# Kernel tuning notes

Hardware: AMD Instinct MI355X
Metric: run time of the kernel (lower is better)

## Reference

```python
import jax, jax.numpy as jnp
import numpy as np

HEADS = 8
HEAD_DIM = 64
SCALE = HEAD_DIM ** -0.5


def setup_inputs() -> dict:
    key = jax.random.key(0)
    ks = jax.random.split(key, 5)
    d_model, inner = 1024, HEADS * HEAD_DIM  # 512
    x = jax.random.normal(ks[0], (2, 2048, d_model), dtype=jnp.float32)
    # torch Linear weights stored pre-transposed as [in, out]
    Wq = jax.random.normal(ks[1], (d_model, inner), dtype=jnp.float32) * (d_model ** -0.5)
    Wkv = jax.random.normal(ks[2], (d_model, 2 * inner), dtype=jnp.float32) * (d_model ** -0.5)
    Wo = jax.random.normal(ks[3], (inner, d_model), dtype=jnp.float32) * (inner ** -0.5)
    bo = jnp.zeros((d_model,), dtype=jnp.float32)
    return {"x": x, "Wq": Wq, "Wkv": Wkv, "Wo": Wo, "bo": bo}


def reference(x, Wq, Wkv, Wo, bo):
    b, n, _ = x.shape
    q = x @ Wq                       # [b, n, h*d]
    kv = x @ Wkv                     # [b, n, 2*h*d] (self-attention: context = x)
    k, v = jnp.split(kv, 2, axis=-1)

    def split_heads(t):
        return t.reshape(b, n, HEADS, HEAD_DIM).transpose(0, 2, 1, 3)  # [b, h, n, d]

    q, k, v = map(split_heads, (q, k, v))
    sim = jnp.einsum('bhid,bhjd->bhij', q, k) * SCALE  # [b, h, n, n]
    attn = jax.nn.softmax(sim, axis=-1)                # dropout p=0.0 -> identity
    out = jnp.einsum('bhij,bhjd->bhid', attn, v)       # [b, h, n, d]
    out = out.transpose(0, 2, 1, 3).reshape(b, n, HEADS * HEAD_DIM)
    return out @ Wo + bo
```

## Files before the change

### kernel.cpp

```cpp
#include <hip/hip_runtime.h>

typedef _Float16 f16;
typedef __attribute__((ext_vector_type(4))) _Float16 f16x4;
typedef __attribute__((ext_vector_type(8))) _Float16 f16x8;
typedef __attribute__((ext_vector_type(4))) float f32x4;

#define CEXP 0.18033688011112042f
#define QKB_LD 1056

__device__ __forceinline__ void gload16(const f16* g, f16* l) {
    __builtin_amdgcn_global_load_lds((const __attribute__((address_space(1))) void*)g,
                                     (__attribute__((address_space(3))) void*)l, 16, 0, 0);
}

__global__ __launch_bounds__(256) void conv_f32_f16_k(const float* __restrict__ in,
                                                      f16* __restrict__ out) {
    int idx = (blockIdx.x * 256 + threadIdx.x) * 8;
    float4 a = *(const float4*)(in + idx);
    float4 b = *(const float4*)(in + idx + 4);
    f16x8 o;
    o[0] = (f16)a.x; o[1] = (f16)a.y; o[2] = (f16)a.z; o[3] = (f16)a.w;
    o[4] = (f16)b.x; o[5] = (f16)b.y; o[6] = (f16)b.z; o[7] = (f16)b.w;
    *(f16x8*)(out + idx) = o;
}

__global__ __launch_bounds__(256) void transpose_conv_k(const float* __restrict__ in,
                                                        f16* __restrict__ out,
                                                        int N, int ldo, int row_off) {
    __shared__ float tile[32][33];
    int tx = threadIdx.x & 31, ty = threadIdx.x >> 5;
    int n0 = blockIdx.x * 32, k0 = blockIdx.y * 32;
#pragma unroll
    for (int j = 0; j < 4; j++)
        tile[ty + j * 8][tx] = in[(size_t)(k0 + ty + j * 8) * N + n0 + tx];
    __syncthreads();
#pragma unroll
    for (int j = 0; j < 4; j++)
        out[(size_t)(row_off + n0 + ty + j * 8) * ldo + k0 + tx] = (f16)tile[tx][ty + j * 8];
}

template <int MODE, int BN>
__global__ __launch_bounds__(256) void gemm_k(
    const f16* __restrict__ A, const f16* __restrict__ Bt,
    f16* __restrict__ Cqk, f16* __restrict__ Cvt,
    float* __restrict__ Cout, const float* __restrict__ bias,
    int K, int NTILES) {
    __shared__ __align__(16) f16 As[128 * 64];
    __shared__ __align__(16) f16 Bs[BN * 64];
    constexpr int MI = (BN == 128) ? 4 : 2;
    int bid = blockIdx.x;
    int nt = bid % NTILES, mt = bid / NTILES;
    int m0 = mt * 128, n0 = nt * BN;
    int tid = threadIdx.x;
    int lane = tid & 63, w = tid >> 6;
    int rowBase = (BN == 128) ? (w >> 1) * 64 : w * 32;
    int colBase = (BN == 128) ? (w & 1) * 64 : 0;
    int lr = lane & 15, lg = lane >> 4;
    int rowL = lane >> 3;
    int colL = (lane & 7) * 8;
    int bRow0 = (BN == 128) ? w * 32 : w * 16;
    const f16* aSrc = A + (size_t)(m0 + w * 32 + rowL) * K + colL;
    const f16* bSrc = Bt + (size_t)(n0 + bRow0 + rowL) * K + colL;
    f32x4 acc[MI][4] = {};

    for (int k0 = 0; k0 < K; k0 += 64) {
#pragma unroll
        for (int j = 0; j < 4; j++)
            gload16(aSrc + k0 + (size_t)(j * 8) * K, &As[(w * 32 + j * 8) * 64]);
#pragma unroll
        for (int j = 0; j < (BN == 128 ? 4 : 2); j++)
            gload16(bSrc + k0 + (size_t)(j * 8) * K, &Bs[(bRow0 + j * 8) * 64]);
        __syncthreads();
#pragma unroll
        for (int ks = 0; ks < 2; ks++) {
            f16x8 af[MI], bf[4];
#pragma unroll
            for (int i = 0; i < MI; i++)
                af[i] = *(const f16x8*)(&As[(rowBase + i * 16 + lr) * 64 + ks * 32 + lg * 8]);
#pragma unroll
            for (int j = 0; j < 4; j++)
                bf[j] = *(const f16x8*)(&Bs[(colBase + j * 16 + lr) * 64 + ks * 32 + lg * 8]);
#pragma unroll
            for (int i = 0; i < MI; i++)
#pragma unroll
                for (int j = 0; j < 4; j++)
                    acc[i][j] = __builtin_amdgcn_mfma_f32_16x16x32_f16(af[i], bf[j], acc[i][j], 0, 0, 0);
        }
        __syncthreads();
    }

#pragma unroll
    for (int i = 0; i < MI; i++) {
#pragma unroll
        for (int j = 0; j < 4; j++) {
            int row = m0 + rowBase + i * 16 + lg * 4;
            int col = n0 + colBase + j * 16 + lr;
            if (MODE == 1) {
                float bv = bias[col];
#pragma unroll
                for (int r = 0; r < 4; r++)
                    Cout[(size_t)(row + r) * 1024 + col] = acc[i][j][r] + bv;
            } else {
                if (col < 1024) {
                    float sc = (col < 512) ? CEXP : 1.0f;
#pragma unroll
                    for (int r = 0; r < 4; r++)
                        Cqk[(size_t)(row + r) * QKB_LD + col] = (f16)(acc[i][j][r] * sc);
                } else {
                    int c = col - 1024;
                    int hh = c >> 6, d = c & 63;
                    int bb = row >> 11, n = row & 2047;
                    int pr = bb * 8 + hh;
                    int tt = n >> 6, kvl = n & 63;
                    int kg = kvl >> 4, lga = (kvl >> 2) & 3;
                    int dgp = d >> 5, dh = (d >> 4) & 1, lra = d & 15;
                    f16x4 ov;
#pragma unroll
                    for (int r = 0; r < 4; r++) ov[r] = (f16)acc[i][j][r];
                    size_t idx = ((((size_t)(pr * 32 + tt) * 4 + kg) * 2 + dgp) * 64
                                  + lga * 16 + lra) * 8 + dh * 4;
                    *(f16x4*)(Cvt + idx) = ov;
                }
            }
        }
    }
}

__global__ __launch_bounds__(512, 4) void attn_k(const f16* __restrict__ qkb,
                                                 const f16* __restrict__ vt2,
                                                 f16* __restrict__ ao) {
    __shared__ __align__(16) f16 Ks[2][4 * 4096];

    int bid = blockIdx.x;
    int xcd = bid & 7;
    int pair = xcd * 2 + ((bid >> 3) & 1);
    int qblk = bid >> 4;
    int b = pair >> 3, h = pair & 7;
    int tid = threadIdx.x;
    int lane = tid & 63, w = tid >> 6;
    int half = w >> 2, wl = w & 3;
    int lr = lane & 15, lg = lane >> 4;
    int q0 = qblk * 64 + wl * 16;

    const f16* qb = qkb + (size_t)b * 2048 * QKB_LD + h * 64;
    const f16* kb = qb + 512;

    f16x8 qf0 = *(const f16x8*)(qb + (size_t)(q0 + lr) * QKB_LD + lg * 8);
    f16x8 qf1 = *(const f16x8*)(qb + (size_t)(q0 + lr) * QKB_LD + 32 + lg * 8);

    int srcCol = (((lane & 7) ^ (lane >> 3)) << 3);
    int rowL = lane >> 3;
    const f16* ksrc = kb + (size_t)(half * 1024 + wl * 16 + rowL) * QKB_LD + srcCol;
    const f16* vbase = vt2 + ((size_t)pair * 32) * 4096 + lane * 8;

    auto stageK = [&](int buf, int tt) {
        f16* dst = &Ks[half][buf * 4096 + (wl * 16) * 64];
        gload16(ksrc + (size_t)(tt * 64) * QKB_LD, dst);
        gload16(ksrc + (size_t)(tt * 64 + 8) * QKB_LD, dst + 8 * 64);
    };

    stageK(0, 0); stageK(1, 1); stageK(2, 2);
    asm volatile("s_waitcnt vmcnt(2)" ::: "memory");
    __builtin_amdgcn_s_barrier();
    asm volatile("" ::: "memory");

    int kOffA = (lg * 8) ^ ((lr & 7) << 3);

    f32x4 acc[4] = {};
    float m = -INFINITY, lp = 0.f;
    f32x4 sA[4], sB[4];

    {
        __builtin_amdgcn_s_setprio(1);
#pragma unroll
        for (int kg = 0; kg < 4; kg++) {
            const f16* krow = &Ks[half][(kg * 16 + lr) * 64];
            f16x8 ka0 = *(const f16x8*)(krow + kOffA);
            f16x8 ka1 = *(const f16x8*)(krow + (kOffA ^ 32));
            f32x4 z = {};
            z = __builtin_amdgcn_mfma_f32_16x16x32_f16(ka0, qf0, z, 0, 0, 0);
            sA[kg] = __builtin_amdgcn_mfma_f32_16x16x32_f16(ka1, qf1, z, 0, 0, 0);
        }
        __builtin_amdgcn_s_setprio(0);
    }

    auto body = [&](f32x4 (&sCur)[4], f32x4 (&sNxt)[4], int t) {
        const f16* vl = vbase + (size_t)(half * 16 + t) * 4096;
        f16x8 vv[8];
#pragma unroll
        for (int i = 0; i < 8; i++) vv[i] = *(const f16x8*)(vl + i * 512);

        if (t <= 12) stageK((t + 3) & 3, t + 3);

        if (t < 15) {
            const f16* kbuf = &Ks[half][((t + 1) & 3) * 4096];
            __builtin_amdgcn_s_setprio(1);
#pragma unroll
            for (int kg = 0; kg < 4; kg++) {
                const f16* krow = kbuf + (kg * 16 + lr) * 64;
                f16x8 ka0 = *(const f16x8*)(krow + kOffA);
                f16x8 ka1 = *(const f16x8*)(krow + (kOffA ^ 32));
                f32x4 z = {};
                z = __builtin_amdgcn_mfma_f32_16x16x32_f16(ka0, qf0, z, 0, 0, 0);
                sNxt[kg] = __builtin_amdgcn_mfma_f32_16x16x32_f16(ka1, qf1, z, 0, 0, 0);
            }
            __builtin_amdgcn_s_setprio(0);
        }

        float x0 = fmaxf(fmaxf(sCur[0][0], sCur[0][1]), fmaxf(sCur[0][2], sCur[0][3]));
        float x1 = fmaxf(fmaxf(sCur[1][0], sCur[1][1]), fmaxf(sCur[1][2], sCur[1][3]));
        float x2 = fmaxf(fmaxf(sCur[2][0], sCur[2][1]), fmaxf(sCur[2][2], sCur[2][3]));
        float x3 = fmaxf(fmaxf(sCur[3][0], sCur[3][1]), fmaxf(sCur[3][2], sCur[3][3]));
        float ownmx = fmaxf(fmaxf(x0, x1), fmaxf(x2, x3));
        if (!__all(ownmx - m <= 8.f)) {
            float mx = fmaxf(ownmx, __shfl_xor(ownmx, 16, 64));
            mx = fmaxf(mx, __shfl_xor(mx, 32, 64));
            float mn = fmaxf(m, mx);
            float alpha = __builtin_amdgcn_exp2f(m - mn);
            m = mn;
            lp *= alpha;
#pragma unroll
            for (int dg = 0; dg < 4; dg++)
#pragma unroll
                for (int r = 0; r < 4; r++) acc[dg][r] *= alpha;
        }
        f16x4 pf[4];
#pragma unroll
        for (int kg = 0; kg < 4; kg++) {
            float p0 = __builtin_amdgcn_exp2f(sCur[kg][0] - m);
            float p1 = __builtin_amdgcn_exp2f(sCur[kg][1] - m);
            float p2 = __builtin_amdgcn_exp2f(sCur[kg][2] - m);
            float p3 = __builtin_amdgcn_exp2f(sCur[kg][3] - m);
            pf[kg][0] = (f16)p0; pf[kg][1] = (f16)p1;
            pf[kg][2] = (f16)p2; pf[kg][3] = (f16)p3;
            lp += (p0 + p1) + (p2 + p3);
        }

        __builtin_amdgcn_s_setprio(1);
#pragma unroll
        for (int kg = 0; kg < 4; kg++)
#pragma unroll
            for (int dgp = 0; dgp < 2; dgp++) {
                f16x8 vx = vv[kg * 2 + dgp];
                f16x4 vlo = __builtin_shufflevector(vx, vx, 0, 1, 2, 3);
                f16x4 vhi = __builtin_shufflevector(vx, vx, 4, 5, 6, 7);
                acc[dgp * 2]     = __builtin_amdgcn_mfma_f32_16x16x16f16(vlo, pf[kg], acc[dgp * 2], 0, 0, 0);
                acc[dgp * 2 + 1] = __builtin_amdgcn_mfma_f32_16x16x16f16(vhi, pf[kg], acc[dgp * 2 + 1], 0, 0, 0);
            }
        __builtin_amdgcn_s_setprio(0);

        if (t <= 12)      { asm volatile("s_waitcnt vmcnt(2)" ::: "memory"); }
        else if (t == 13) { asm volatile("s_waitcnt vmcnt(0)" ::: "memory"); }
        if (t < 15) {
            __builtin_amdgcn_s_barrier();
            asm volatile("" ::: "memory");
        }
    };

    for (int u = 0; u < 8; u++) {
        body(sA, sB, 2 * u);
        body(sB, sA, 2 * u + 1);
    }

    lp += __shfl_xor(lp, 16, 64);
    lp += __shfl_xor(lp, 32, 64);
    __syncthreads();
    float* mO = (float*)&Ks[0][0];
    float* mL = mO + 4 * 64 * 16;
    float* mM = mL + 4 * 64;
    if (half == 1) {
#pragma unroll
        for (int dg = 0; dg < 4; dg++)
            *(f32x4*)&mO[(wl * 64 + lane) * 16 + dg * 4] = acc[dg];
        mL[wl * 64 + lane] = lp;
        mM[wl * 64 + lane] = m;
    }
    __syncthreads();
    if (half == 0) {
        float mP = mM[wl * 64 + lane];
        float lpP = mL[wl * 64 + lane];
        float M = fmaxf(m, mP);
        float a = __builtin_amdgcn_exp2f(m - M);
        float c = __builtin_amdgcn_exp2f(mP - M);
        float inv = 1.f / (lp * a + lpP * c);
#pragma unroll
        for (int dg = 0; dg < 4; dg++) {
            f32x4 oP = *(const f32x4*)&mO[(wl * 64 + lane) * 16 + dg * 4];
            f16x4 ov;
#pragma unroll
            for (int r = 0; r < 4; r++)
                ov[r] = (f16)((acc[dg][r] * a + oP[r] * c) * inv);
            *(f16x4*)(ao + (size_t)(b * 2048 + q0 + lr) * 512 + h * 64 + dg * 16 + lg * 4) = ov;
        }
    }
}

extern "C" void kernel_launch(void* const* d_in, const int* in_sizes, int n_in,
                              void* d_out, int out_size, void* d_ws, size_t ws_size,
                              hipStream_t stream) {
    const float* x   = (const float*)d_in[0];
    const float* Wq  = (const float*)d_in[1];
    const float* Wkv = (const float*)d_in[2];
    const float* Wo  = (const float*)d_in[3];
    const float* bo  = (const float*)d_in[4];
    float* out = (float*)d_out;

    f16* xb    = (f16*)d_ws;
    f16* wqkvT = xb + 4096 * 1024;
    f16* woT   = wqkvT + 1536 * 1024;
    f16* qkb   = woT + 1024 * 512;
    f16* vtb2  = qkb + 4096 * QKB_LD;
    f16* ao    = vtb2 + 16 * 32 * 4096;

    conv_f32_f16_k<<<2048, 256, 0, stream>>>(x, xb);
    transpose_conv_k<<<dim3(16, 32), 256, 0, stream>>>(Wq, wqkvT, 512, 1024, 0);
    transpose_conv_k<<<dim3(32, 32), 256, 0, stream>>>(Wkv, wqkvT, 1024, 1024, 512);
    transpose_conv_k<<<dim3(32, 16), 256, 0, stream>>>(Wo, woT, 1024, 512, 0);

    gemm_k<0, 64><<<32 * 24, 256, 0, stream>>>(xb, wqkvT, qkb, vtb2, nullptr, nullptr, 1024, 24);
    attn_k<<<512, 512, 0, stream>>>(qkb, vtb2, ao);
    gemm_k<1, 128><<<32 * 8, 256, 0, stream>>>(ao, woT, nullptr, nullptr, out, bo, 512, 8);
}
```

Baseline: 92.34 us.

## Double-buffer GEMM LDS tiles and restructure attention K staging into 128-row blocks

The GEMM kernel gets double-buffered LDS tiles, so the next K-slice loads while the current one is multiplied. This hides global-to-LDS latency behind MFMA work. The attention kernel replaces its 4-deep 64-row K ring and software-pipelined QK^T with a 2-buffer scheme that stages 128 keys per iteration and computes both 64-key score blocks up front. That halves the number of barriers, but it drops the cross-iteration overlap of QK^T with softmax, relies on __syncthreads (full vmcnt waits) and raises register pressure.

Result: slower. 96.89 us (+4.9%).

```diff
diff --git a/kernel.cpp b/kernel.cpp
--- a/kernel.cpp
+++ b/kernel.cpp
@@ -45,9 +45,10 @@
     f16* __restrict__ Cqk, f16* __restrict__ Cvt,
     float* __restrict__ Cout, const float* __restrict__ bias,
     int K, int NTILES) {
-    __shared__ __align__(16) f16 As[128 * 64];
-    __shared__ __align__(16) f16 Bs[BN * 64];
+    __shared__ __align__(16) f16 As[2][128 * 64];
+    __shared__ __align__(16) f16 Bs[2][BN * 64];
     constexpr int MI = (BN == 128) ? 4 : 2;
+    constexpr int NB = (BN == 128) ? 4 : 2;
     int bid = blockIdx.x;
     int nt = bid % NTILES, mt = bid / NTILES;
     int m0 = mt * 128, n0 = nt * BN;
@@ -63,23 +64,31 @@
     const f16* bSrc = Bt + (size_t)(n0 + bRow0 + rowL) * K + colL;
     f32x4 acc[MI][4] = {};
 
-    for (int k0 = 0; k0 < K; k0 += 64) {
+    auto stage = [&](int buf, int k0) {
 #pragma unroll
         for (int j = 0; j < 4; j++)
-            gload16(aSrc + k0 + (size_t)(j * 8) * K, &As[(w * 32 + j * 8) * 64]);
-#pragma unroll
-        for (int j = 0; j < (BN == 128 ? 4 : 2); j++)
-            gload16(bSrc + k0 + (size_t)(j * 8) * K, &Bs[(bRow0 + j * 8) * 64]);
-        __syncthreads();
+            gload16(aSrc + k0 + (size_t)(j * 8) * K, &As[buf][(w * 32 + j * 8) * 64]);
+#pragma unroll
+        for (int j = 0; j < NB; j++)
+            gload16(bSrc + k0 + (size_t)(j * 8) * K, &Bs[buf][(bRow0 + j * 8) * 64]);
+    };
+
+    stage(0, 0);
+    __syncthreads();
+
+    int KT = K >> 6;
+    for (int kt = 0; kt < KT; kt++) {
+        int cur = kt & 1;
+        if (kt + 1 < KT) stage(cur ^ 1, (kt + 1) * 64);
 #pragma unroll
         for (int ks = 0; ks < 2; ks++) {
             f16x8 af[MI], bf[4];
 #pragma unroll
             for (int i = 0; i < MI; i++)
-                af[i] = *(const f16x8*)(&As[(rowBase + i * 16 + lr) * 64 + ks * 32 + lg * 8]);
+                af[i] = *(const f16x8*)(&As[cur][(rowBase + i * 16 + lr) * 64 + ks * 32 + lg * 8]);
 #pragma unroll
             for (int j = 0; j < 4; j++)
-                bf[j] = *(const f16x8*)(&Bs[(colBase + j * 16 + lr) * 64 + ks * 32 + lg * 8]);
+                bf[j] = *(const f16x8*)(&Bs[cur][(colBase + j * 16 + lr) * 64 + ks * 32 + lg * 8]);
 #pragma unroll
             for (int i = 0; i < MI; i++)
 #pragma unroll
@@ -129,7 +138,7 @@
 __global__ __launch_bounds__(512, 4) void attn_k(const f16* __restrict__ qkb,
                                                  const f16* __restrict__ vt2,
                                                  f16* __restrict__ ao) {
-    __shared__ __align__(16) f16 Ks[2][4 * 4096];
+    __shared__ __align__(16) f16 Ks[2][2][128 * 64];
 
     int bid = blockIdx.x;
     int xcd = bid & 7;
@@ -150,67 +159,61 @@
 
     int srcCol = (((lane & 7) ^ (lane >> 3)) << 3);
     int rowL = lane >> 3;
-    const f16* ksrc = kb + (size_t)(half * 1024 + wl * 16 + rowL) * QKB_LD + srcCol;
+    const f16* ksrc = kb + (size_t)(half * 1024 + wl * 32 + rowL) * QKB_LD + srcCol;
     const f16* vbase = vt2 + ((size_t)pair * 32) * 4096 + lane * 8;
 
     auto stageK = [&](int buf, int tt) {
-        f16* dst = &Ks[half][buf * 4096 + (wl * 16) * 64];
-        gload16(ksrc + (size_t)(tt * 64) * QKB_LD, dst);
-        gload16(ksrc + (size_t)(tt * 64 + 8) * QKB_LD, dst + 8 * 64);
+        f16* dst = &Ks[half][buf][(wl * 32) * 64];
+        const f16* s = ksrc + (size_t)(tt * 128) * QKB_LD;
+#pragma unroll
+        for (int j = 0; j < 4; j++)
+            gload16(s + (size_t)(j * 8) * QKB_LD, dst + (j * 8) * 64);
     };
 
-    stageK(0, 0); stageK(1, 1); stageK(2, 2);
-    asm volatile("s_waitcnt vmcnt(2)" ::: "memory");
-    __builtin_amdgcn_s_barrier();
-    asm volatile("" ::: "memory");
+    stageK(0, 0);
+    __syncthreads();
 
     int kOffA = (lg * 8) ^ ((lr & 7) << 3);
 
     f32x4 acc[4] = {};
     float m = -INFINITY, lp = 0.f;
-    f32x4 sA[4], sB[4];
-
-    {
+
+    for (int t = 0; t < 8; t++) {
+        int cur = t & 1;
+
+        const f16* vl1 = vbase + (size_t)(half * 16 + 2 * t) * 4096;
+        f16x8 vv1[8];
+#pragma unroll
+        for (int i = 0; i < 8; i++) vv1[i] = *(const f16x8*)(vl1 + i * 512);
+
+        if (t < 7) stageK(cur ^ 1, t + 1);
+
+        f32x4 s1[4], s2[4];
         __builtin_amdgcn_s_setprio(1);
 #pragma unroll
         for (int kg = 0; kg < 4; kg++) {
-            const f16* krow = &Ks[half][(kg * 16 + lr) * 64];
+            const f16* krow = &Ks[half][cur][(kg * 16 + lr) * 64];
             f16x8 ka0 = *(const f16x8*)(krow + kOffA);
             f16x8 ka1 = *(const f16x8*)(krow + (kOffA ^ 32));
             f32x4 z = {};
             z = __builtin_amdgcn_mfma_f32_16x16x32_f16(ka0, qf0, z, 0, 0, 0);
-            sA[kg] = __builtin_amdgcn_mfma_f32_16x16x32_f16(ka1, qf1, z, 0, 0, 0);
+            s1[kg] = __builtin_amdgcn_mfma_f32_16x16x32_f16(ka1, qf1, z, 0, 0, 0);
+        }
+#pragma unroll
+        for (int kg = 0; kg < 4; kg++) {
+            const f16* krow = &Ks[half][cur][(64 + kg * 16 + lr) * 64];
+            f16x8 ka0 = *(const f16x8*)(krow + kOffA);
+            f16x8 ka1 = *(const f16x8*)(krow + (kOffA ^ 32));
+            f32x4 z = {};
+            z = __builtin_amdgcn_mfma_f32_16x16x32_f16(ka0, qf0, z, 0, 0, 0);
+            s2[kg] = __builtin_amdgcn_mfma_f32_16x16x32_f16(ka1, qf1, z, 0, 0, 0);
         }
         __builtin_amdgcn_s_setprio(0);
-    }
-
-    auto body = [&](f32x4 (&sCur)[4], f32x4 (&sNxt)[4], int t) {
-        const f16* vl = vbase + (size_t)(half * 16 + t) * 4096;
-        f16x8 vv[8];
-#pragma unroll
-        for (int i = 0; i < 8; i++) vv[i] = *(const f16x8*)(vl + i * 512);
-
-        if (t <= 12) stageK((t + 3) & 3, t + 3);
-
-        if (t < 15) {
-            const f16* kbuf = &Ks[half][((t + 1) & 3) * 4096];
-            __builtin_amdgcn_s_setprio(1);
-#pragma unroll
-            for (int kg = 0; kg < 4; kg++) {
-                const f16* krow = kbuf + (kg * 16 + lr) * 64;
-                f16x8 ka0 = *(const f16x8*)(krow + kOffA);
-                f16x8 ka1 = *(const f16x8*)(krow + (kOffA ^ 32));
-                f32x4 z = {};
-                z = __builtin_amdgcn_mfma_f32_16x16x32_f16(ka0, qf0, z, 0, 0, 0);
-                sNxt[kg] = __builtin_amdgcn_mfma_f32_16x16x32_f16(ka1, qf1, z, 0, 0, 0);
-            }
-            __builtin_amdgcn_s_setprio(0);
-        }
-
-        float x0 = fmaxf(fmaxf(sCur[0][0], sCur[0][1]), fmaxf(sCur[0][2], sCur[0][3]));
-        float x1 = fmaxf(fmaxf(sCur[1][0], sCur[1][1]), fmaxf(sCur[1][2], sCur[1][3]));
-        float x2 = fmaxf(fmaxf(sCur[2][0], sCur[2][1]), fmaxf(sCur[2][2], sCur[2][3]));
-        float x3 = fmaxf(fmaxf(sCur[3][0], sCur[3][1]), fmaxf(sCur[3][2], sCur[3][3]));
+
+        float x0 = fmaxf(fmaxf(s1[0][0], s1[0][1]), fmaxf(s1[0][2], s1[0][3]));
+        float x1 = fmaxf(fmaxf(s1[1][0], s1[1][1]), fmaxf(s1[1][2], s1[1][3]));
+        float x2 = fmaxf(fmaxf(s1[2][0], s1[2][1]), fmaxf(s1[2][2], s1[2][3]));
+        float x3 = fmaxf(fmaxf(s1[3][0], s1[3][1]), fmaxf(s1[3][2], s1[3][3]));
         float ownmx = fmaxf(fmaxf(x0, x1), fmaxf(x2, x3));
         if (!__all(ownmx - m <= 8.f)) {
             float mx = fmaxf(ownmx, __shfl_xor(ownmx, 16, 64));
@@ -224,48 +227,85 @@
 #pragma unroll
                 for (int r = 0; r < 4; r++) acc[dg][r] *= alpha;
         }
-        f16x4 pf[4];
+        f16x4 pf1[4];
 #pragma unroll
         for (int kg = 0; kg < 4; kg++) {
-            float p0 = __builtin_amdgcn_exp2f(sCur[kg][0] - m);
-            float p1 = __builtin_amdgcn_exp2f(sCur[kg][1] - m);
-            float p2 = __builtin_amdgcn_exp2f(sCur[kg][2] - m);
-            float p3 = __builtin_amdgcn_exp2f(sCur[kg][3] - m);
-            pf[kg][0] = (f16)p0; pf[kg][1] = (f16)p1;
-            pf[kg][2] = (f16)p2; pf[kg][3] = (f16)p3;
+            float p0 = __builtin_amdgcn_exp2f(s1[kg][0] - m);
+            float p1 = __builtin_amdgcn_exp2f(s1[kg][1] - m);
+            float p2 = __builtin_amdgcn_exp2f(s1[kg][2] - m);
+            float p3 = __builtin_amdgcn_exp2f(s1[kg][3] - m);
+            pf1[kg][0] = (f16)p0; pf1[kg][1] = (f16)p1;
+            pf1[kg][2] = (f16)p2; pf1[kg][3] = (f16)p3;
             lp += (p0 + p1) + (p2 + p3);
         }
 
+        const f16* vl2 = vl1 + 4096;
+        f16x8 vv2[8];
+#pragma unroll
+        for (int i = 0; i < 8; i++) vv2[i] = *(const f16x8*)(vl2 + i * 512);
+
         __builtin_amdgcn_s_setprio(1);
 #pragma unroll
         for (int kg = 0; kg < 4; kg++)
 #pragma unroll
             for (int dgp = 0; dgp < 2; dgp++) {
-                f16x8 vx = vv[kg * 2 + dgp];
+                f16x8 vx = vv1[kg * 2 + dgp];
                 f16x4 vlo = __builtin_shufflevector(vx, vx, 0, 1, 2, 3);
                 f16x4 vhi = __builtin_shufflevector(vx, vx, 4, 5, 6, 7);
-                acc[dgp * 2]     = __builtin_amdgcn_mfma_f32_16x16x16f16(vlo, pf[kg], acc[dgp * 2], 0, 0, 0);
-                acc[dgp * 2 + 1] = __builtin_amdgcn_mfma_f32_16x16x16f16(vhi, pf[kg], acc[dgp * 2 + 1], 0, 0, 0);
+                acc[dgp * 2]     = __builtin_amdgcn_mfma_f32_16x16x16f16(vlo, pf1[kg], acc[dgp * 2], 0, 0, 0);
+                acc[dgp * 2 + 1] = __builtin_amdgcn_mfma_f32_16x16x16f16(vhi, pf1[kg], acc[dgp * 2 + 1], 0, 0, 0);
             }
         __builtin_amdgcn_s_setprio(0);
 
-        if (t <= 12)      { asm volatile("s_waitcnt vmcnt(2)" ::: "memory"); }
-        else if (t == 13) { asm volatile("s_waitcnt vmcnt(0)" ::: "memory"); }
-        if (t < 15) {
-            __builtin_amdgcn_s_barrier();
-            asm volatile("" ::: "memory");
-        }
-    };
-
-    for (int u = 0; u < 8; u++) {
-        body(sA, sB, 2 * u);
-        body(sB, sA, 2 * u + 1);
+        float y0 = fmaxf(fmaxf(s2[0][0], s2[0][1]), fmaxf(s2[0][2], s2[0][3]));
+        float y1 = fmaxf(fmaxf(s2[1][0], s2[1][1]), fmaxf(s2[1][2], s2[1][3]));
+        float y2 = fmaxf(fmaxf(s2[2][0], s2[2][1]), fmaxf(s2[2][2], s2[2][3]));
+        float y3 = fmaxf(fmaxf(s2[3][0], s2[3][1]), fmaxf(s2[3][2], s2[3][3]));
+        float ownmx2 = fmaxf(fmaxf(y0, y1), fmaxf(y2, y3));
+        if (!__all(ownmx2 - m <= 8.f)) {
+            float mx = fmaxf(ownmx2, __shfl_xor(ownmx2, 16, 64));
+            mx = fmaxf(mx, __shfl_xor(mx, 32, 64));
+            float mn = fmaxf(m, mx);
+            float alpha = __builtin_amdgcn_exp2f(m - mn);
+            m = mn;
+            lp *= alpha;
+#pragma unroll
+            for (int dg = 0; dg < 4; dg++)
+#pragma unroll
+                for (int r = 0; r < 4; r++) acc[dg][r] *= alpha;
+        }
+        f16x4 pf2[4];
+#pragma unroll
+        for (int kg = 0; kg < 4; kg++) {
+            float p0 = __builtin_amdgcn_exp2f(s2[kg][0] - m);
+            float p1 = __builtin_amdgcn_exp2f(s2[kg][1] - m);
+            float p2 = __builtin_amdgcn_exp2f(s2[kg][2] - m);
+            float p3 = __builtin_amdgcn_exp2f(s2[kg][3] - m);
+            pf2[kg][0] = (f16)p0; pf2[kg][1] = (f16)p1;
+            pf2[kg][2] = (f16)p2; pf2[kg][3] = (f16)p3;
+            lp += (p0 + p1) + (p2 + p3);
+        }
+
+        __builtin_amdgcn_s_setprio(1);
+#pragma unroll
+        for (int kg = 0; kg < 4; kg++)
+#pragma unroll
+            for (int dgp = 0; dgp < 2; dgp++) {
+                f16x8 vx = vv2[kg * 2 + dgp];
+                f16x4 vlo = __builtin_shufflevector(vx, vx, 0, 1, 2, 3);
+                f16x4 vhi = __builtin_shufflevector(vx, vx, 4, 5, 6, 7);
+                acc[dgp * 2]     = __builtin_amdgcn_mfma_f32_16x16x16f16(vlo, pf2[kg], acc[dgp * 2], 0, 0, 0);
+                acc[dgp * 2 + 1] = __builtin_amdgcn_mfma_f32_16x16x16f16(vhi, pf2[kg], acc[dgp * 2 + 1], 0, 0, 0);
+            }
+        __builtin_amdgcn_s_setprio(0);
+
+        if (t < 7) __syncthreads();
     }
 
     lp += __shfl_xor(lp, 16, 64);
     lp += __shfl_xor(lp, 32, 64);
     __syncthreads();
-    float* mO = (float*)&Ks[0][0];
+    float* mO = (float*)&Ks[0][0][0];
     float* mL = mO + 4 * 64 * 16;
     float* mM = mL + 4 * 64;
     if (half == 1) {
```
